# Performance work log

Hardware: AMD Instinct MI355X
Metric: run time of the kernel (lower is better)

Reference implementation:

```python
import jax, jax.numpy as jnp
import numpy as np

N_NODES = 20000
L_MAX = 6
R_IN = 256
R_HID = 512
R_OUT = 256
LEAKY_SLOPE = 0.01  # torch.nn.functional.leaky_relu default


def setup_inputs() -> dict:
    key = jax.random.key(0)
    k1, k2, k3, k4 = jax.random.split(key, 4)
    x = jax.random.normal(k1, (N_NODES, R_IN, L_MAX * 2), dtype=jnp.float32)
    # per-node rotation angles -> per-degree 2x2 rotation matrices (k*theta for degree k)
    theta = jax.random.uniform(k2, (N_NODES,), dtype=jnp.float32, minval=0.0, maxval=2.0 * np.pi)
    ang = theta[:, None] * jnp.arange(1, L_MAX + 1, dtype=jnp.float32)[None, :]  # (n, L)
    c, s = jnp.cos(ang), jnp.sin(ang)
    rot_theta = jnp.stack([jnp.stack([c, -s], axis=-1),
                           jnp.stack([s, c], axis=-1)], axis=-2)  # (n, L, 2, 2)
    # xavier_normal: std = sqrt(2 / (fan_in + fan_out))
    W1 = jax.random.normal(k3, (L_MAX, R_HID, R_IN), dtype=jnp.float32) * np.sqrt(2.0 / (R_IN + R_HID))
    W2 = jax.random.normal(k4, (L_MAX, R_OUT, R_HID), dtype=jnp.float32) * np.sqrt(2.0 / (R_HID + R_OUT))
    return {"x": x, "rot_theta": rot_theta, "W1": W1, "W2": W2}


def so2_linear(x, W, r_out):
    # x: (n, r_in, L_max*2); W: (L_max, r_out, r_in)
    n = x.shape[0]
    x4 = x.reshape(n, -1, L_MAX, 2)              # (n, r_in, L, 2)
    out = jnp.einsum('nilc,loi->nolc', x4, W)    # fused block-diagonal GEMM over degrees
    return out.reshape(n, r_out, L_MAX * 2)


def rot_activation(x, rot):
    # rotate each degree-l 2-vector into local frame, apply leaky_relu, rotate back
    n = x.shape[0]
    x4 = x.reshape(n, -1, L_MAX, 2)                      # (n, r, L, 2)
    a = jnp.einsum('njlm,nlmc->njlc', x4, rot)           # x @ R per (node, degree)
    a = jnp.where(a >= 0, a, LEAKY_SLOPE * a)            # pointwise leaky_relu
    out = jnp.einsum('njlc,nlmc->njlm', a, rot)          # (act) @ R^T  (inverse rotation)
    return out.reshape(x.shape)


def reference(x, rot_theta, W1, W2):
    h = so2_linear(x, W1, R_HID)
    h = rot_activation(h, rot_theta)
    return so2_linear(h, W2, R_OUT)
```

## Files before the change

kernel.cpp:

```cpp
#include <hip/hip_runtime.h>
#include <stdint.h>


#define LMAX 6
#define NN 20000
#define RIN 256
#define RHID 512
#define ROUT 256
#define MTILE 128
#define NTILES 313
#define MPAD (NTILES*MTILE)

typedef __attribute__((ext_vector_type(8))) short short8;
typedef __attribute__((ext_vector_type(16))) float f32x16;

__device__ __forceinline__ uint16_t f2bf(float f) {
  uint32_t x = __builtin_bit_cast(uint32_t, f);
  x += 0x7fffu + ((x >> 16) & 1u);
  return (uint16_t)(x >> 16);
}
__device__ __forceinline__ float bf2f(uint16_t u) {
  return __builtin_bit_cast(float, ((uint32_t)u) << 16);
}
__device__ __forceinline__ float lrelu(float v) {
  return v >= 0.f ? v : 0.01f * v;
}
__device__ __forceinline__ uint32_t pk2(float a, float b) {
  return (uint32_t)f2bf(a) | ((uint32_t)f2bf(b) << 16);
}

__device__ __forceinline__ f32x16 mfma32(short8 a, short8 b, f32x16 c) {
  return __builtin_amdgcn_mfma_f32_32x32x16_bf16(a, b, c, 0, 0, 0);
}

__device__ __forceinline__ int swz512(int row, int colb) {
  return row * 512 + ((((colb >> 4) ^ row) & 31) << 4) + (colb & 15);
}

__global__ void prep_weights(const float* __restrict__ W1, const float* __restrict__ W2,
                             uint16_t* __restrict__ w1f, uint16_t* __restrict__ w2f) {
  int idx = blockIdx.x * 256 + threadIdx.x;
  if (idx >= LMAX * RHID * RIN) return;
  {
    int l = idx / (RHID * RIN);
    int rem = idx - l * (RHID * RIN);
    int o = rem >> 8;
    int i = rem & 255;
    int lane = ((i >> 3) & 1) * 32 + (o & 31);
    size_t dst = (size_t)l * (RHID * RIN) +
                 ((((size_t)(o >> 5) * 16 + (i >> 4)) * 64 + lane) * 8 + (i & 7));
    w1f[dst] = f2bf(W1[idx]);
  }
  {
    int l = idx / (ROUT * RHID);
    int rem = idx - l * (ROUT * RHID);
    int o = rem >> 9;
    int j = rem & 511;
    int lane = ((j >> 3) & 1) * 32 + (o & 31);
    size_t dst = (size_t)l * (ROUT * RHID) +
                 ((((size_t)(o >> 5) * 32 + (j >> 4)) * 64 + lane) * 8 + (j & 7));
    w2f[dst] = f2bf(W2[idx]);
  }
}

__global__ void prep_x(const float* __restrict__ x, const float* __restrict__ rot,
                       uint16_t* __restrict__ xr) {
  int t = blockIdx.x * 256 + threadIdx.x;
  if (t >= NN * RIN) return;
  int n = t >> 8, i = t & 255;
  const float4* xp = (const float4*)(x + (size_t)t * 12);
  float4 v0 = xp[0], v1 = xp[1], v2 = xp[2];
  float xv[12] = {v0.x, v0.y, v0.z, v0.w, v1.x, v1.y, v1.z, v1.w, v2.x, v2.y, v2.z, v2.w};
  const float* rp = rot + (size_t)n * 24;
#pragma unroll
  for (int l = 0; l < LMAX; ++l) {
    float c0 = xv[2 * l], c1 = xv[2 * l + 1];
    float r00 = rp[4 * l + 0], r01 = rp[4 * l + 1];
    float r10 = rp[4 * l + 2], r11 = rp[4 * l + 3];
    float a0 = c0 * r00 + c1 * r10;
    float a1 = c0 * r01 + c1 * r11;
    size_t base = (size_t)l * MPAD * RIN + (size_t)(2 * n) * RIN + i;
    xr[base] = f2bf(a0);
    xr[base + RIN] = f2bf(a1);
  }
}

__global__ __launch_bounds__(512, 2) void so2_gemm(
    const uint16_t* __restrict__ xr,
    const uint16_t* __restrict__ w1f,
    const uint16_t* __restrict__ w2f,
    uint16_t* __restrict__ g) {
  __shared__ alignas(16) uint8_t Xs[MTILE * 512];
  __shared__ alignas(16) uint8_t A2[MTILE * 512];

  const int tile = blockIdx.x;
  const int l = blockIdx.y;
  const int m0 = tile * MTILE;
  const int tid = threadIdx.x;
  const int lane = tid & 63;
  const int wid = tid >> 6;
  const int l31 = lane & 31;
  const int lh = lane >> 5;
  const int wm = wid & 1;
  const int wn = wid >> 1;

  const uint16_t* w1p = w1f + (size_t)l * (RHID * RIN);
  const uint16_t* w2p = w2f + (size_t)l * (ROUT * RHID);

  const char* xsrc = (const char*)(xr + (size_t)l * MPAD * RIN + (size_t)m0 * RIN);
#pragma unroll
  for (int it = 0; it < 8; ++it) {
    int off = it * 8192 + tid * 16;
    int row = off >> 9;
    int colb = off & 511;
    short8 v = __builtin_nontemporal_load((const short8*)(xsrc + off));
    *(short8*)(Xs + swz512(row, colb)) = v;
  }
  __syncthreads();

  f32x16 acc1[2][2];
  f32x16 acc2[2][2];
#pragma unroll
  for (int a = 0; a < 2; ++a)
#pragma unroll
    for (int b = 0; b < 2; ++b) acc2[a][b] = (f32x16)(0.f);

  auto G1 = [&](int oc) {
#pragma unroll
    for (int a = 0; a < 2; ++a)
#pragma unroll
      for (int b = 0; b < 2; ++b) acc1[a][b] = (f32x16)(0.f);
    const uint16_t* wb0 = w1p + (size_t)(oc * 8 + wn * 2) * (16 * 64 * 8);
    const uint16_t* wb1 = wb0 + 16 * 64 * 8;
#pragma unroll 4
    for (int ks = 0; ks < 16; ++ks) {
      short8 a0 = *(const short8*)(wb0 + ((size_t)ks * 64 + lane) * 8);
      short8 a1 = *(const short8*)(wb1 + ((size_t)ks * 64 + lane) * 8);
#pragma unroll
      for (int mbi = 0; mbi < 2; ++mbi) {
        short8 b = *(const short8*)(Xs + swz512((wm * 2 + mbi) * 32 + l31,
                                                ks * 32 + lh * 16));
        acc1[0][mbi] = mfma32(a0, b, acc1[0][mbi]);
        acc1[1][mbi] = mfma32(a1, b, acc1[1][mbi]);
      }
    }
  };

  auto WA2 = [&]() {
#pragma unroll
    for (int fi = 0; fi < 2; ++fi)
#pragma unroll
      for (int mbi = 0; mbi < 2; ++mbi) {
        int mrow = (wm * 2 + mbi) * 32 + l31;
#pragma unroll
        for (int q = 0; q < 4; ++q) {
          uint2 pv;
          pv.x = pk2(lrelu(acc1[fi][mbi][4 * q + 0]), lrelu(acc1[fi][mbi][4 * q + 1]));
          pv.y = pk2(lrelu(acc1[fi][mbi][4 * q + 2]), lrelu(acc1[fi][mbi][4 * q + 3]));
          int colb = (wn * 2 + fi) * 64 + q * 16 + lh * 8;
          *(uint2*)(A2 + swz512(mrow, colb)) = pv;
        }
      }
  };

  auto G2 = [&](int oc) {
#pragma unroll 4
    for (int ks = 0; ks < 16; ++ks) {
      short8 b0 = *(const short8*)(A2 + swz512((wm * 2) * 32 + l31, ks * 32 + lh * 16));
      short8 b1 = *(const short8*)(A2 + swz512((wm * 2 + 1) * 32 + l31, ks * 32 + lh * 16));
#pragma unroll
      for (int foi = 0; foi < 2; ++foi) {
        short8 a = *(const short8*)(w2p +
            ((size_t)((wn * 2 + foi) * 32 + oc * 16 + ks) * 64 + lane) * 8);
        acc2[foi][0] = mfma32(a, b0, acc2[foi][0]);
        acc2[foi][1] = mfma32(a, b1, acc2[foi][1]);
      }
    }
  };

  G1(0);
  WA2();
  __syncthreads();

  {
#pragma unroll
    for (int a = 0; a < 2; ++a)
#pragma unroll
      for (int b = 0; b < 2; ++b) acc1[a][b] = (f32x16)(0.f);
    const uint16_t* wb0 = w1p + (size_t)(8 + wn * 2) * (16 * 64 * 8);
    const uint16_t* wb1 = wb0 + 16 * 64 * 8;
#pragma unroll 2
    for (int ks = 0; ks < 16; ++ks) {
      short8 b20 = *(const short8*)(A2 + swz512((wm * 2) * 32 + l31, ks * 32 + lh * 16));
      short8 b21 = *(const short8*)(A2 + swz512((wm * 2 + 1) * 32 + l31, ks * 32 + lh * 16));
#pragma unroll
      for (int foi = 0; foi < 2; ++foi) {
        short8 a = *(const short8*)(w2p +
            ((size_t)((wn * 2 + foi) * 32 + ks) * 64 + lane) * 8);
        acc2[foi][0] = mfma32(a, b20, acc2[foi][0]);
        acc2[foi][1] = mfma32(a, b21, acc2[foi][1]);
      }
      short8 a10 = *(const short8*)(wb0 + ((size_t)ks * 64 + lane) * 8);
      short8 a11 = *(const short8*)(wb1 + ((size_t)ks * 64 + lane) * 8);
#pragma unroll
      for (int mbi = 0; mbi < 2; ++mbi) {
        short8 b = *(const short8*)(Xs + swz512((wm * 2 + mbi) * 32 + l31,
                                                ks * 32 + lh * 16));
        acc1[0][mbi] = mfma32(a10, b, acc1[0][mbi]);
        acc1[1][mbi] = mfma32(a11, b, acc1[1][mbi]);
      }
    }
  }
  __syncthreads();
  WA2();
  __syncthreads();
  G2(1);
  __syncthreads();

#pragma unroll
  for (int foi = 0; foi < 2; ++foi)
#pragma unroll
    for (int mbi = 0; mbi < 2; ++mbi) {
      int mrow = (wm * 2 + mbi) * 32 + l31;
#pragma unroll
      for (int q = 0; q < 4; ++q) {
        uint2 pv;
        pv.x = pk2(acc2[foi][mbi][4 * q + 0], acc2[foi][mbi][4 * q + 1]);
        pv.y = pk2(acc2[foi][mbi][4 * q + 2], acc2[foi][mbi][4 * q + 3]);
        int colb = (wn * 2 + foi) * 64 + q * 16 + lh * 8;
        *(uint2*)(Xs + swz512(mrow, colb)) = pv;
      }
    }
  __syncthreads();

  char* gdst = (char*)(g + (size_t)l * MPAD * ROUT + (size_t)m0 * ROUT);
#pragma unroll
  for (int it = 0; it < 8; ++it) {
    int off = it * 8192 + tid * 16;
    int row = off >> 9;
    int colb = off & 511;
    short8 v = *(const short8*)(Xs + swz512(row, colb));
    __builtin_nontemporal_store(v, (short8*)(gdst + off));
  }
}

__global__ void post_out(const uint16_t* __restrict__ g, const float* __restrict__ rot,
                         float* __restrict__ out) {
  int n = blockIdx.x;
  int o = threadIdx.x;
  const float* rp = rot + (size_t)n * 24;
  float res[12];
#pragma unroll
  for (int l = 0; l < LMAX; ++l) {
    size_t base = (size_t)l * MPAD * ROUT + (size_t)(2 * n) * ROUT + o;
    float g0 = bf2f(g[base]);
    float g1 = bf2f(g[base + ROUT]);
    res[2 * l]     = rp[4 * l + 0] * g0 + rp[4 * l + 1] * g1;
    res[2 * l + 1] = rp[4 * l + 2] * g0 + rp[4 * l + 3] * g1;
  }
  float4* op = (float4*)(out + (size_t)(n * 256 + o) * 12);
  op[0] = make_float4(res[0], res[1], res[2], res[3]);
  op[1] = make_float4(res[4], res[5], res[6], res[7]);
  op[2] = make_float4(res[8], res[9], res[10], res[11]);
}

extern "C" void kernel_launch(void* const* d_in, const int* in_sizes, int n_in,
                              void* d_out, int out_size, void* d_ws, size_t ws_size,
                              hipStream_t stream) {
  (void)in_sizes; (void)n_in; (void)out_size;
  const float* x   = (const float*)d_in[0];
  const float* rot = (const float*)d_in[1];
  const float* W1  = (const float*)d_in[2];
  const float* W2  = (const float*)d_in[3];
  float* out = (float*)d_out;

  const size_t xr_elems = (size_t)LMAX * MPAD * RIN;
  const size_t w_elems  = (size_t)LMAX * RHID * RIN;
  if (ws_size < (size_t)LMAX * MPAD * ROUT * 2) return;

  uint16_t* xr  = (uint16_t*)d_out;
  uint16_t* w1f = xr + xr_elems;
  uint16_t* w2f = w1f + w_elems;
  uint16_t* g   = (uint16_t*)d_ws;

  prep_weights<<<3072, 256, 0, stream>>>(W1, W2, w1f, w2f);
  prep_x<<<20000, 256, 0, stream>>>(x, rot, xr);
  dim3 gg(NTILES, LMAX);
  so2_gemm<<<gg, 512, 0, stream>>>(xr, w1f, w2f, g);
  post_out<<<20000, 256, 0, stream>>>(g, rot, out);
}
```

Before: 360.0 us.

## Halve GEMM M-tile to 64 rows with 4 waves and use hardware bf16 pack

The fused two-layer GEMM now uses 64-row tiles and 256-thread blocks, so each wave covers all rows and a distinct column slice and the wm/wn wave split is removed. This doubles the tile count, giving more blocks for occupancy and load balance, but each block loads W1/W2 fragments for only 64 rows, which halves weight reuse per global load. The manual bf16 round-and-pack is also replaced with the v_cvt_pk_bf16_f32 instruction to cut ALU work in the epilogues.

```diff
diff --git a/kernel.cpp b/kernel.cpp
--- a/kernel.cpp
+++ b/kernel.cpp
@@ -7,8 +7,8 @@
 #define RIN 256
 #define RHID 512
 #define ROUT 256
-#define MTILE 128
-#define NTILES 313
+#define MTILE 64
+#define NTILES 626
 #define MPAD (NTILES*MTILE)
 
 typedef __attribute__((ext_vector_type(8))) short short8;
@@ -25,8 +25,10 @@
 __device__ __forceinline__ float lrelu(float v) {
   return v >= 0.f ? v : 0.01f * v;
 }
-__device__ __forceinline__ uint32_t pk2(float a, float b) {
-  return (uint32_t)f2bf(a) | ((uint32_t)f2bf(b) << 16);
+__device__ __forceinline__ uint32_t cvtpk(float a, float b) {
+  uint32_t r;
+  asm("v_cvt_pk_bf16_f32 %0, %1, %2" : "=v"(r) : "v"(a), "v"(b));
+  return r;
 }
 
 __device__ __forceinline__ f32x16 mfma32(short8 a, short8 b, f32x16 c) {
@@ -85,7 +87,7 @@
   }
 }
 
-__global__ __launch_bounds__(512, 2) void so2_gemm(
+__global__ __launch_bounds__(256, 2) void so2_gemm(
     const uint16_t* __restrict__ xr,
     const uint16_t* __restrict__ w1f,
     const uint16_t* __restrict__ w2f,
@@ -101,8 +103,6 @@
   const int wid = tid >> 6;
   const int l31 = lane & 31;
   const int lh = lane >> 5;
-  const int wm = wid & 1;
-  const int wn = wid >> 1;
 
   const uint16_t* w1p = w1f + (size_t)l * (RHID * RIN);
   const uint16_t* w2p = w2f + (size_t)l * (ROUT * RHID);
@@ -110,7 +110,7 @@
   const char* xsrc = (const char*)(xr + (size_t)l * MPAD * RIN + (size_t)m0 * RIN);
 #pragma unroll
   for (int it = 0; it < 8; ++it) {
-    int off = it * 8192 + tid * 16;
+    int off = it * 4096 + tid * 16;
     int row = off >> 9;
     int colb = off & 511;
     short8 v = __builtin_nontemporal_load((const short8*)(xsrc + off));
@@ -130,18 +130,17 @@
     for (int a = 0; a < 2; ++a)
 #pragma unroll
       for (int b = 0; b < 2; ++b) acc1[a][b] = (f32x16)(0.f);
-    const uint16_t* wb0 = w1p + (size_t)(oc * 8 + wn * 2) * (16 * 64 * 8);
+    const uint16_t* wb0 = w1p + (size_t)(oc * 8 + wid * 2) * (16 * 64 * 8);
     const uint16_t* wb1 = wb0 + 16 * 64 * 8;
 #pragma unroll 4
     for (int ks = 0; ks < 16; ++ks) {
       short8 a0 = *(const short8*)(wb0 + ((size_t)ks * 64 + lane) * 8);
       short8 a1 = *(const short8*)(wb1 + ((size_t)ks * 64 + lane) * 8);
 #pragma unroll
-      for (int mbi = 0; mbi < 2; ++mbi) {
-        short8 b = *(const short8*)(Xs + swz512((wm * 2 + mbi) * 32 + l31,
-                                                ks * 32 + lh * 16));
-        acc1[0][mbi] = mfma32(a0, b, acc1[0][mbi]);
-        acc1[1][mbi] = mfma32(a1, b, acc1[1][mbi]);
+      for (int mb = 0; mb < 2; ++mb) {
+        short8 b = *(const short8*)(Xs + swz512(mb * 32 + l31, ks * 32 + lh * 16));
+        acc1[0][mb] = mfma32(a0, b, acc1[0][mb]);
+        acc1[1][mb] = mfma32(a1, b, acc1[1][mb]);
       }
     }
   };
@@ -150,14 +149,14 @@
 #pragma unroll
     for (int fi = 0; fi < 2; ++fi)
 #pragma unroll
-      for (int mbi = 0; mbi < 2; ++mbi) {
-        int mrow = (wm * 2 + mbi) * 32 + l31;
+      for (int mb = 0; mb < 2; ++mb) {
+        int mrow = mb * 32 + l31;
 #pragma unroll
         for (int q = 0; q < 4; ++q) {
           uint2 pv;
-          pv.x = pk2(lrelu(acc1[fi][mbi][4 * q + 0]), lrelu(acc1[fi][mbi][4 * q + 1]));
-          pv.y = pk2(lrelu(acc1[fi][mbi][4 * q + 2]), lrelu(acc1[fi][mbi][4 * q + 3]));
-          int colb = (wn * 2 + fi) * 64 + q * 16 + lh * 8;
+          pv.x = cvtpk(lrelu(acc1[fi][mb][4 * q + 0]), lrelu(acc1[fi][mb][4 * q + 1]));
+          pv.y = cvtpk(lrelu(acc1[fi][mb][4 * q + 2]), lrelu(acc1[fi][mb][4 * q + 3]));
+          int colb = (wid * 2 + fi) * 64 + q * 16 + lh * 8;
           *(uint2*)(A2 + swz512(mrow, colb)) = pv;
         }
       }
@@ -166,12 +165,12 @@
   auto G2 = [&](int oc) {
 #pragma unroll 4
     for (int ks = 0; ks < 16; ++ks) {
-      short8 b0 = *(const short8*)(A2 + swz512((wm * 2) * 32 + l31, ks * 32 + lh * 16));
-      short8 b1 = *(const short8*)(A2 + swz512((wm * 2 + 1) * 32 + l31, ks * 32 + lh * 16));
+      short8 b0 = *(const short8*)(A2 + swz512(l31, ks * 32 + lh * 16));
+      short8 b1 = *(const short8*)(A2 + swz512(32 + l31, ks * 32 + lh * 16));
 #pragma unroll
       for (int foi = 0; foi < 2; ++foi) {
         short8 a = *(const short8*)(w2p +
-            ((size_t)((wn * 2 + foi) * 32 + oc * 16 + ks) * 64 + lane) * 8);
+            ((size_t)((wid * 2 + foi) * 32 + oc * 16 + ks) * 64 + lane) * 8);
         acc2[foi][0] = mfma32(a, b0, acc2[foi][0]);
         acc2[foi][1] = mfma32(a, b1, acc2[foi][1]);
       }
@@ -187,27 +186,26 @@
     for (int a = 0; a < 2; ++a)
 #pragma unroll
       for (int b = 0; b < 2; ++b) acc1[a][b] = (f32x16)(0.f);
-    const uint16_t* wb0 = w1p + (size_t)(8 + wn * 2) * (16 * 64 * 8);
+    const uint16_t* wb0 = w1p + (size_t)(8 + wid * 2) * (16 * 64 * 8);
     const uint16_t* wb1 = wb0 + 16 * 64 * 8;
 #pragma unroll 2
     for (int ks = 0; ks < 16; ++ks) {
-      short8 b20 = *(const short8*)(A2 + swz512((wm * 2) * 32 + l31, ks * 32 + lh * 16));
-      short8 b21 = *(const short8*)(A2 + swz512((wm * 2 + 1) * 32 + l31, ks * 32 + lh * 16));
+      short8 b20 = *(const short8*)(A2 + swz512(l31, ks * 32 + lh * 16));
+      short8 b21 = *(const short8*)(A2 + swz512(32 + l31, ks * 32 + lh * 16));
 #pragma unroll
       for (int foi = 0; foi < 2; ++foi) {
         short8 a = *(const short8*)(w2p +
-            ((size_t)((wn * 2 + foi) * 32 + ks) * 64 + lane) * 8);
+            ((size_t)((wid * 2 + foi) * 32 + ks) * 64 + lane) * 8);
         acc2[foi][0] = mfma32(a, b20, acc2[foi][0]);
         acc2[foi][1] = mfma32(a, b21, acc2[foi][1]);
       }
       short8 a10 = *(const short8*)(wb0 + ((size_t)ks * 64 + lane) * 8);
       short8 a11 = *(const short8*)(wb1 + ((size_t)ks * 64 + lane) * 8);
 #pragma unroll
-      for (int mbi = 0; mbi < 2; ++mbi) {
-        short8 b = *(const short8*)(Xs + swz512((wm * 2 + mbi) * 32 + l31,
-                                                ks * 32 + lh * 16));
-        acc1[0][mbi] = mfma32(a10, b, acc1[0][mbi]);
-        acc1[1][mbi] = mfma32(a11, b, acc1[1][mbi]);
+      for (int mb = 0; mb < 2; ++mb) {
+        short8 b = *(const short8*)(Xs + swz512(mb * 32 + l31, ks * 32 + lh * 16));
+        acc1[0][mb] = mfma32(a10, b, acc1[0][mb]);
+        acc1[1][mb] = mfma32(a11, b, acc1[1][mb]);
       }
     }
   }
@@ -220,14 +218,14 @@
 #pragma unroll
   for (int foi = 0; foi < 2; ++foi)
 #pragma unroll
-    for (int mbi = 0; mbi < 2; ++mbi) {
-      int mrow = (wm * 2 + mbi) * 32 + l31;
+    for (int mb = 0; mb < 2; ++mb) {
+      int mrow = mb * 32 + l31;
 #pragma unroll
       for (int q = 0; q < 4; ++q) {
         uint2 pv;
-        pv.x = pk2(acc2[foi][mbi][4 * q + 0], acc2[foi][mbi][4 * q + 1]);
-        pv.y = pk2(acc2[foi][mbi][4 * q + 2], acc2[foi][mbi][4 * q + 3]);
-        int colb = (wn * 2 + foi) * 64 + q * 16 + lh * 8;
+        pv.x = cvtpk(acc2[foi][mb][4 * q + 0], acc2[foi][mb][4 * q + 1]);
+        pv.y = cvtpk(acc2[foi][mb][4 * q + 2], acc2[foi][mb][4 * q + 3]);
+        int colb = (wid * 2 + foi) * 64 + q * 16 + lh * 8;
         *(uint2*)(Xs + swz512(mrow, colb)) = pv;
       }
     }
@@ -236,7 +234,7 @@
   char* gdst = (char*)(g + (size_t)l * MPAD * ROUT + (size_t)m0 * ROUT);
 #pragma unroll
   for (int it = 0; it < 8; ++it) {
-    int off = it * 8192 + tid * 16;
+    int off = it * 4096 + tid * 16;
     int row = off >> 9;
     int colb = off & 511;
     short8 v = *(const short8*)(Xs + swz512(row, colb));
@@ -286,6 +284,6 @@
   prep_weights<<<3072, 256, 0, stream>>>(W1, W2, w1f, w2f);
   prep_x<<<20000, 256, 0, stream>>>(x, rot, xr);
   dim3 gg(NTILES, LMAX);
-  so2_gemm<<<gg, 512, 0, stream>>>(xr, w1f, w2f, g);
+  so2_gemm<<<gg, 256, 0, stream>>>(xr, w1f, w2f, g);
   post_out<<<20000, 256, 0, stream>>>(g, rot, out);
 }
```

Result: faster. 337.7 us (-6.2%).
